# Kernel optimization log

Hardware: AMD Instinct MI355X
Metric: run time of the kernel (lower is better)

## Reference

```python
import jax, jax.numpy as jnp
import numpy as np

SCALE = 8.0  # sqrt(head_dim=64)


def setup_inputs() -> dict:
    key = jax.random.key(0)
    k1, k2, k3, k4 = jax.random.split(key, 4)
    B, Lq, Lk, H, C, K = 2, 4096, 4096, 8, 64, 32
    return {
        "query": jax.random.normal(k1, (B, Lq, H, C), dtype=jnp.float32),
        "key": jax.random.normal(k2, (B, Lk, H, C), dtype=jnp.float32),
        "value": jax.random.normal(k3, (B, Lk, H, C), dtype=jnp.float32),
        "pos": jax.random.randint(k4, (B, Lq, H, K), 0, Lk, dtype=jnp.int64),
    }


def reference(query, key, value, pos):
    # query: [B, Lq, H, C]; key/value: [B, Lk, H, C]; pos: [B, Lq, H, K]
    B, Lq, H, C = query.shape
    b_idx = jnp.arange(B)[:, None, None, None]   # [B,1,1,1]
    h_idx = jnp.arange(H)[None, None, :, None]   # [1,1,H,1]
    # gather along sequence dim per (batch, head): -> [B, Lq, H, K, C]
    k = key[b_idx, pos, h_idx, :]
    v = value[b_idx, pos, h_idx, :]
    # per-query attention over K gathered keys
    score = jnp.einsum("blhc,blhkc->blhk", query, k) / SCALE
    attn = jax.nn.softmax(score, axis=-1)
    out = jnp.einsum("blhk,blhkc->blhc", attn, v)
    return out
```

## Files before the change

kernel.cpp:

```cpp
#include <hip/hip_runtime.h>
#include <math.h>

constexpr int B  = 2;
constexpr int Lq = 4096;
constexpr int Lk = 4096;
constexpr int H  = 8;
constexpr int C  = 64;
constexpr int K  = 32;
constexpr float INV_SCALE = 0.125f;

__global__ __launch_bounds__(256) void topk_attn_kernel(
    const float* __restrict__ query,
    const float* __restrict__ key,
    const float* __restrict__ value,
    const int*   __restrict__ pos,
    float*       __restrict__ out)
{
    const int bid    = blockIdx.x;
    const int group  = bid & 15;
    const int lchunk = bid >> 4;
    const int wave   = threadIdx.x >> 6;
    const int lane   = threadIdx.x & 63;
    const int g      = lane >> 4;
    const int c4     = lane & 15;

    const int b = group >> 3;
    const int h = group & 7;
    const int l = lchunk * 4 + wave;

    const size_t row  = ((size_t)(b * Lq + l) * H + h);
    const size_t qoff = row * (size_t)C;

    float4 q4 = *(const float4*)(query + qoff + 4 * c4);
    q4.x *= INV_SCALE; q4.y *= INV_SCALE; q4.z *= INV_SCALE; q4.w *= INV_SCALE;

    const int p = pos[row * K + (lane & 31)];

    const float* kbase = key   + (size_t)b * Lk * H * C + (size_t)h * C;
    const float* vbase = value + (size_t)b * Lk * H * C + (size_t)h * C;

    int off[8];
    #pragma unroll
    for (int i = 0; i < 8; ++i) {
        const int pk = __shfl(p, 4 * i + g);
        off[i] = pk * (H * C) + 4 * c4;
    }

    float s[8];
    #pragma unroll
    for (int i = 0; i < 8; ++i) {
        const float4 kv = *(const float4*)(kbase + off[i]);
        float t = q4.x * kv.x;
        t = fmaf(q4.y, kv.y, t);
        t = fmaf(q4.z, kv.z, t);
        t = fmaf(q4.w, kv.w, t);
        #pragma unroll
        for (int m = 8; m >= 1; m >>= 1) t += __shfl_xor(t, m);
        s[i] = t;
    }

    float mx = s[0];
    #pragma unroll
    for (int i = 1; i < 8; ++i) mx = fmaxf(mx, s[i]);
    mx = fmaxf(mx, __shfl_xor(mx, 16));
    mx = fmaxf(mx, __shfl_xor(mx, 32));

    float se = 0.0f;
    #pragma unroll
    for (int i = 0; i < 8; ++i) { s[i] = __expf(s[i] - mx); se += s[i]; }
    se += __shfl_xor(se, 16);
    se += __shfl_xor(se, 32);
    const float inv = 1.0f / se;

    float4 acc = make_float4(0.f, 0.f, 0.f, 0.f);
    #pragma unroll
    for (int i = 0; i < 8; ++i) {
        const float a = s[i] * inv;
        const float4 v4 = *(const float4*)(vbase + off[i]);
        acc.x = fmaf(a, v4.x, acc.x);
        acc.y = fmaf(a, v4.y, acc.y);
        acc.z = fmaf(a, v4.z, acc.z);
        acc.w = fmaf(a, v4.w, acc.w);
    }
    #pragma unroll
    for (int m = 16; m <= 32; m <<= 1) {
        acc.x += __shfl_xor(acc.x, m);
        acc.y += __shfl_xor(acc.y, m);
        acc.z += __shfl_xor(acc.z, m);
        acc.w += __shfl_xor(acc.w, m);
    }

    if (g == 0) *(float4*)(out + qoff + 4 * c4) = acc;
}

extern "C" void kernel_launch(void* const* d_in, const int* in_sizes, int n_in,
                              void* d_out, int out_size, void* d_ws, size_t ws_size,
                              hipStream_t stream) {
    const float* query = (const float*)d_in[0];
    const float* key   = (const float*)d_in[1];
    const float* value = (const float*)d_in[2];
    const int*   pos   = (const int*)d_in[3];
    float* out = (float*)d_out;

    const int total_rows = B * Lq * H;
    const int blocks = total_rows / 4;
    topk_attn_kernel<<<blocks, 256, 0, stream>>>(query, key, value, pos, out);
}
```

Measured before the change: 55.91 us.

## Map one query row per 16-lane group instead of one per wave

Each 16-lane group now handles a full query row and loops over all 32 gathered keys, so a block of 256 threads covers 16 rows and the grid shrinks by four. This removes the cross-group shuffle reductions for the softmax and the output accumulation and the redundant query loads, and every lane now stores output. In exchange each lane issues more sequential dependent gathers and shuffles per row, so there is less parallelism per row and longer serial chains.

Measured after the change: 72.68 us. 30.0% more time.

```diff
diff --git a/kernel.cpp b/kernel.cpp
--- a/kernel.cpp
+++ b/kernel.cpp
@@ -8,6 +8,7 @@
 constexpr int C  = 64;
 constexpr int K  = 32;
 constexpr float INV_SCALE = 0.125f;
+constexpr int HC = H * C;
 
 __global__ __launch_bounds__(256) void topk_attn_kernel(
     const float* __restrict__ query,
@@ -26,7 +27,7 @@
 
     const int b = group >> 3;
     const int h = group & 7;
-    const int l = lchunk * 4 + wave;
+    const int l = lchunk * 16 + wave * 4 + g;
 
     const size_t row  = ((size_t)(b * Lq + l) * H + h);
     const size_t qoff = row * (size_t)C;
@@ -34,63 +35,50 @@
     float4 q4 = *(const float4*)(query + qoff + 4 * c4);
     q4.x *= INV_SCALE; q4.y *= INV_SCALE; q4.z *= INV_SCALE; q4.w *= INV_SCALE;
 
-    const int p = pos[row * K + (lane & 31)];
+    const int2 pp = *(const int2*)(pos + row * (size_t)K + 2 * c4);
 
-    const float* kbase = key   + (size_t)b * Lk * H * C + (size_t)h * C;
-    const float* vbase = value + (size_t)b * Lk * H * C + (size_t)h * C;
+    const float* kbase = key   + (size_t)b * Lk * HC + (size_t)h * C;
+    const float* vbase = value + (size_t)b * Lk * HC + (size_t)h * C;
+    const int gbase = g << 4;
 
-    int off[8];
+    float s0 = 0.0f, s1 = 0.0f;
     #pragma unroll
-    for (int i = 0; i < 8; ++i) {
-        const int pk = __shfl(p, 4 * i + g);
-        off[i] = pk * (H * C) + 4 * c4;
-    }
-
-    float s[8];
-    #pragma unroll
-    for (int i = 0; i < 8; ++i) {
-        const float4 kv = *(const float4*)(kbase + off[i]);
+    for (int i = 0; i < K; ++i) {
+        const int pk = __shfl((i & 1) ? pp.y : pp.x, gbase + (i >> 1));
+        const float4 kv = *(const float4*)(kbase + pk * HC + 4 * c4);
         float t = q4.x * kv.x;
         t = fmaf(q4.y, kv.y, t);
         t = fmaf(q4.z, kv.z, t);
         t = fmaf(q4.w, kv.w, t);
         #pragma unroll
         for (int m = 8; m >= 1; m >>= 1) t += __shfl_xor(t, m);
-        s[i] = t;
+        if (c4 == (i & 15)) { if (i < 16) s0 = t; else s1 = t; }
     }
 
-    float mx = s[0];
+    float mx = fmaxf(s0, s1);
     #pragma unroll
-    for (int i = 1; i < 8; ++i) mx = fmaxf(mx, s[i]);
-    mx = fmaxf(mx, __shfl_xor(mx, 16));
-    mx = fmaxf(mx, __shfl_xor(mx, 32));
-
-    float se = 0.0f;
+    for (int m = 8; m >= 1; m >>= 1) mx = fmaxf(mx, __shfl_xor(mx, m));
+    float e0 = __expf(s0 - mx);
+    float e1 = __expf(s1 - mx);
+    float se = e0 + e1;
     #pragma unroll
-    for (int i = 0; i < 8; ++i) { s[i] = __expf(s[i] - mx); se += s[i]; }
-    se += __shfl_xor(se, 16);
-    se += __shfl_xor(se, 32);
+    for (int m = 8; m >= 1; m >>= 1) se += __shfl_xor(se, m);
     const float inv = 1.0f / se;
+    e0 *= inv; e1 *= inv;
 
     float4 acc = make_float4(0.f, 0.f, 0.f, 0.f);
     #pragma unroll
-    for (int i = 0; i < 8; ++i) {
-        const float a = s[i] * inv;
-        const float4 v4 = *(const float4*)(vbase + off[i]);
+    for (int i = 0; i < K; ++i) {
+        const int pk = __shfl((i & 1) ? pp.y : pp.x, gbase + (i >> 1));
+        const float a  = __shfl((i < 16) ? e0 : e1, gbase + (i & 15));
+        const float4 v4 = *(const float4*)(vbase + pk * HC + 4 * c4);
         acc.x = fmaf(a, v4.x, acc.x);
         acc.y = fmaf(a, v4.y, acc.y);
         acc.z = fmaf(a, v4.z, acc.z);
         acc.w = fmaf(a, v4.w, acc.w);
     }
-    #pragma unroll
-    for (int m = 16; m <= 32; m <<= 1) {
-        acc.x += __shfl_xor(acc.x, m);
-        acc.y += __shfl_xor(acc.y, m);
-        acc.z += __shfl_xor(acc.z, m);
-        acc.w += __shfl_xor(acc.w, m);
-    }
 
-    if (g == 0) *(float4*)(out + qoff + 4 * c4) = acc;
+    *(float4*)(out + qoff + 4 * c4) = acc;
 }
 
 extern "C" void kernel_launch(void* const* d_in, const int* in_sizes, int n_in,
@@ -103,6 +91,6 @@
     float* out = (float*)d_out;
 
     const int total_rows = B * Lq * H;
-    const int blocks = total_rows / 4;
+    const int blocks = total_rows / 16;
     topk_attn_kernel<<<blocks, 256, 0, stream>>>(query, key, value, pos, out);
 }
```

## Convert K/V to fp16 in workspace and gather half-precision rows

Applied to the files above, without the earlier changes.

Adds a pre-pass that converts key and value tensors to fp16 in the workspace buffer each call. The attention kernel then gathers 8-byte half4 chunks instead of 16-byte float4, halving gather traffic. It falls back to the fp32 kernel when the workspace is too small. This adds a full streaming conversion pass and reduces K/V precision.

Measured after the change: 53.16 us. 4.9% less time.

```diff
diff --git a/kernel.cpp b/kernel.cpp
--- a/kernel.cpp
+++ b/kernel.cpp
@@ -8,8 +8,115 @@
 constexpr int C  = 64;
 constexpr int K  = 32;
 constexpr float INV_SCALE = 0.125f;
-
-__global__ __launch_bounds__(256) void topk_attn_kernel(
+constexpr int HC = H * C;
+constexpr int NKV = B * Lk * H * C;
+
+typedef _Float16 half4_t __attribute__((ext_vector_type(4)));
+
+__global__ __launch_bounds__(256) void convert_kv_f16(
+    const float* __restrict__ key,
+    const float* __restrict__ value,
+    _Float16*    __restrict__ kh,
+    _Float16*    __restrict__ vh)
+{
+    const int n4 = NKV / 4;
+    for (int i = blockIdx.x * blockDim.x + threadIdx.x;
+         i < 2 * n4; i += gridDim.x * blockDim.x) {
+        if (i < n4) {
+            const float4 v = ((const float4*)key)[i];
+            half4_t h = { (_Float16)v.x, (_Float16)v.y, (_Float16)v.z, (_Float16)v.w };
+            ((half4_t*)kh)[i] = h;
+        } else {
+            const float4 v = ((const float4*)value)[i - n4];
+            half4_t h = { (_Float16)v.x, (_Float16)v.y, (_Float16)v.z, (_Float16)v.w };
+            ((half4_t*)vh)[i - n4] = h;
+        }
+    }
+}
+
+__global__ __launch_bounds__(256) void topk_attn_f16(
+    const float*    __restrict__ query,
+    const _Float16* __restrict__ keyh,
+    const _Float16* __restrict__ valh,
+    const int*      __restrict__ pos,
+    float*          __restrict__ out)
+{
+    const int bid    = blockIdx.x;
+    const int group  = bid & 15;
+    const int lchunk = bid >> 4;
+    const int wave   = threadIdx.x >> 6;
+    const int lane   = threadIdx.x & 63;
+    const int g      = lane >> 4;
+    const int c4     = lane & 15;
+
+    const int b = group >> 3;
+    const int h = group & 7;
+    const int l = lchunk * 4 + wave;
+
+    const size_t row  = ((size_t)(b * Lq + l) * H + h);
+    const size_t qoff = row * (size_t)C;
+
+    float4 q4 = *(const float4*)(query + qoff + 4 * c4);
+    q4.x *= INV_SCALE; q4.y *= INV_SCALE; q4.z *= INV_SCALE; q4.w *= INV_SCALE;
+
+    const int p = pos[row * (size_t)K + (lane & 31)];
+
+    const _Float16* kbase = keyh + (size_t)b * Lk * HC + (size_t)h * C;
+    const _Float16* vbase = valh + (size_t)b * Lk * HC + (size_t)h * C;
+
+    int off[8];
+    #pragma unroll
+    for (int i = 0; i < 8; ++i)
+        off[i] = __shfl(p, 4 * i + g) * HC + 4 * c4;
+
+    float s[8];
+    #pragma unroll
+    for (int i = 0; i < 8; ++i) {
+        const half4_t kv = *(const half4_t*)(kbase + off[i]);
+        float t = q4.x * (float)kv.x;
+        t = fmaf(q4.y, (float)kv.y, t);
+        t = fmaf(q4.z, (float)kv.z, t);
+        t = fmaf(q4.w, (float)kv.w, t);
+        #pragma unroll
+        for (int m = 8; m >= 1; m >>= 1) t += __shfl_xor(t, m);
+        s[i] = t;
+    }
+
+    float mx = s[0];
+    #pragma unroll
+    for (int i = 1; i < 8; ++i) mx = fmaxf(mx, s[i]);
+    mx = fmaxf(mx, __shfl_xor(mx, 16));
+    mx = fmaxf(mx, __shfl_xor(mx, 32));
+
+    float se = 0.0f;
+    #pragma unroll
+    for (int i = 0; i < 8; ++i) { s[i] = __expf(s[i] - mx); se += s[i]; }
+    se += __shfl_xor(se, 16);
+    se += __shfl_xor(se, 32);
+    const float inv = 1.0f / se;
+
+    float4 acc = make_float4(0.f, 0.f, 0.f, 0.f);
+    #pragma unroll
+    for (int i = 0; i < 8; ++i) {
+        const float a = s[i] * inv;
+        const half4_t v4 = *(const half4_t*)(vbase + off[i]);
+        acc.x = fmaf(a, (float)v4.x, acc.x);
+        acc.y = fmaf(a, (float)v4.y, acc.y);
+        acc.z = fmaf(a, (float)v4.z, acc.z);
+        acc.w = fmaf(a, (float)v4.w, acc.w);
+    }
+    #pragma unroll
+    for (int m = 16; m <= 32; m <<= 1) {
+        acc.x += __shfl_xor(acc.x, m);
+        acc.y += __shfl_xor(acc.y, m);
+        acc.z += __shfl_xor(acc.z, m);
+        acc.w += __shfl_xor(acc.w, m);
+    }
+
+    if (g == 0) *(float4*)(out + qoff + 4 * c4) = acc;
+}
+
+__global__ __launch_bounds__(256) void topk_attn_f32(
     const float* __restrict__ query,
     const float* __restrict__ key,
     const float* __restrict__ value,
@@ -34,17 +141,15 @@
     float4 q4 = *(const float4*)(query + qoff + 4 * c4);
     q4.x *= INV_SCALE; q4.y *= INV_SCALE; q4.z *= INV_SCALE; q4.w *= INV_SCALE;
 
-    const int p = pos[row * K + (lane & 31)];
-
-    const float* kbase = key   + (size_t)b * Lk * H * C + (size_t)h * C;
-    const float* vbase = value + (size_t)b * Lk * H * C + (size_t)h * C;
+    const int p = pos[row * (size_t)K + (lane & 31)];
+
+    const float* kbase = key   + (size_t)b * Lk * HC + (size_t)h * C;
+    const float* vbase = value + (size_t)b * Lk * HC + (size_t)h * C;
 
     int off[8];
     #pragma unroll
-    for (int i = 0; i < 8; ++i) {
-        const int pk = __shfl(p, 4 * i + g);
-        off[i] = pk * (H * C) + 4 * c4;
-    }
+    for (int i = 0; i < 8; ++i)
+        off[i] = __shfl(p, 4 * i + g) * HC + 4 * c4;
 
     float s[8];
     #pragma unroll
@@ -104,5 +209,14 @@
 
     const int total_rows = B * Lq * H;
     const int blocks = total_rows / 4;
-    topk_attn_kernel<<<blocks, 256, 0, stream>>>(query, key, value, pos, out);
-}
+
+    const size_t need = (size_t)2 * NKV * sizeof(_Float16);
+    if (ws_size >= need && d_ws != nullptr) {
+        _Float16* kh = (_Float16*)d_ws;
+        _Float16* vh = kh + NKV;
+        convert_kv_f16<<<2048, 256, 0, stream>>>(key, value, kh, vh);
+        topk_attn_f16<<<blocks, 256, 0, stream>>>(query, kh, vh, pos, out);
+    } else {
+        topk_attn_f32<<<blocks, 256, 0, stream>>>(query, key, value, pos, out);
+    }
+}
```
